# Performance work log

Measured on AMD Instinct MI355X. Metric: run time of the kernel, lower is better.

The kernel has to match this reference:

```python
import jax, jax.numpy as jnp
import numpy as np

# Param packing order: [capacitance_x, capacitance_y] + for each direction in
# (ax, by, xy, yx, xx, yy): [conductance, mean, std, pot]  -> total 26 scalars.
_DIR = {"ax": 0, "by": 1, "xy": 2, "yx": 3, "xx": 4, "yy": 5}

B, T = 4096, 4096


def setup_inputs() -> dict:
    key = jax.random.key(0)
    inputs = jax.random.normal(key, (B, T, 2), dtype=jnp.float32)
    # initializer constants from the keras layer
    params = jnp.asarray([1.0, 1.0] + [0.001, 0.3, 3.0, 1.0] * 6, dtype=jnp.float32)
    return {"inputs": inputs, "params": params}


def reference(inputs, params):
    cap_x, cap_y = params[0], params[1]

    def syn(d, pre, post):
        i = 2 + 4 * _DIR[d]
        g, mean, std, pot = params[i], params[i + 1], params[i + 2], params[i + 3]
        return g * jax.nn.sigmoid(std * (pre - mean)) * (pot - post)

    def step(state, inp):
        x, y = state                      # each [B, 1]
        a, b = inp[:, :1], inp[:, 1:]     # each [B, 1]
        cur_x = syn("ax", a, x) + syn("yx", y, x) + syn("xx", x, x)
        cur_y = syn("by", b, y) + syn("xy", x, y) + syn("yy", y, y)
        x = x + cur_x / cap_x
        y = y + cur_y / cap_y
        out = jnp.concatenate((x, y), axis=-1)  # [B, 2]
        return (x, y), out

    bsz = inputs.shape[0]
    x0 = jnp.zeros((bsz, 1), inputs.dtype)
    y0 = jnp.ones((bsz, 1), inputs.dtype)   # initial state = concat(zeros, ones)
    _, outs = jax.lax.scan(step, (x0, y0), jnp.swapaxes(inputs, 0, 1))  # [T, B, 2]
    return jnp.swapaxes(outs, 0, 1)  # [B, T, 2]
```

## Files before the change

kernel.cpp:

```cpp
#include <hip/hip_runtime.h>

#define TLEN  4096
#define NROWS 4096
#define RPB   32
#define K     32
#define NC    (TLEN / K)
#define SGSL  (16 * 64)
#define STP   34
#define STSL  (64 * STP)
#define UN    8

__device__ __forceinline__ float fexp2(float x) { return __builtin_amdgcn_exp2f(x); }
__device__ __forceinline__ float frcp(float x)  { return __builtin_amdgcn_rcpf(x); }
__device__ __forceinline__ float sigz(float z)  { return frcp(1.0f + fexp2(z)); }

__device__ __forceinline__ float lane_swap1(float v) {
    int r = __builtin_amdgcn_update_dpp(0, __float_as_int(v), 0xB1, 0xF, 0xF, true);
    return __int_as_float(r);
}

__device__ void run_fast(const float* __restrict__ inp, const float* __restrict__ prm,
                         float* __restrict__ out,
                         float4* __restrict__ sgbuf,
                         float*  __restrict__ st) {
    const int tid  = threadIdx.x;
    const int wid  = tid >> 6;
    const int lane = tid & 63;
    const int R0   = blockIdx.x * RPB;
    const float L2E = 1.4426950408889634f;
    float2* __restrict__ out2 = (float2*)out;

    if (wid == 1) {
        const int row = lane >> 1, dir = lane & 1;
        const float sd = dir ? prm[8] : prm[4];
        const float mn = dir ? prm[7] : prm[3];
        const float c1 = -sd * L2E, c0 = sd * mn * L2E;
        const float gA = dir ? (prm[6] / prm[1]) : (prm[2] / prm[0]);
        const float P  = gA * (dir ? prm[9] : prm[5]);
        const float Gn = -gA;
        const float4* __restrict__ src = (const float4*)inp + (size_t)(R0 + row) * (TLEN / 2);

        auto produce = [&](int c) {
            float4* sl = sgbuf + ((c & 1) ? SGSL : 0);
            const int base = c * 16;
#pragma unroll
            for (int j = 0; j < 16; ++j) {
                float4 v = src[base + j];
                float p0 = dir ? v.y : v.x;
                float p1 = dir ? v.w : v.z;
                float s0 = sigz(__builtin_fmaf(c1, p0, c0));
                float s1 = sigz(__builtin_fmaf(c1, p1, c0));
                float4 o; o.x = Gn * s0; o.y = P * s0;
                          o.z = Gn * s1; o.w = P * s1;
                sl[j * 64 + lane] = o;
            }
        };

        produce(0);
        __syncthreads();
        for (int c = 0; c < NC; ++c) {
            if (c + 1 < NC) produce(c + 1);
            __syncthreads();
        }
    } else if (wid == 2) {
        auto flush = [&](int c) {
            const float* sl = st + ((c & 1) ? STSL : 0);
            const int col = lane & 31;
#pragma unroll
            for (int j = 0; j < 16; ++j) {
                int ro = 2 * j + (lane >> 5);
                float2 v;
                v.x = sl[(2 * ro)     * STP + col];
                v.y = sl[(2 * ro + 1) * STP + col];
                out2[(size_t)(R0 + ro) * TLEN + (size_t)c * K + col] = v;
            }
        };

        __syncthreads();
        for (int c = 0; c < NC; ++c) {
            if (c >= 1) flush(c - 1);
            __syncthreads();
        }
        flush(NC - 1);
    } else {
        const int par = lane & 1;
        const int sfB = par ? 22 : 18, t2B = par ? 10 : 14;
        const float ic  = 1.0f / prm[par];
        const float g1  = prm[sfB] * ic, P1 = g1 * prm[sfB + 3], Gn1 = -g1;
        const float g2  = prm[t2B] * ic, P2 = g2 * prm[t2B + 3], Gn2 = -g2;
        const float sdz = prm[sfB + 2];
        const float c1s = -sdz * L2E, c0s = sdz * prm[sfB + 1] * L2E;

        float x   = par ? 1.0f : 0.0f;
        float sig = sigz(__builtin_fmaf(c1s, x, c0s));
        float u   = __builtin_fmaf(-sig, sig, sig);

        auto resync = [&]() {
            sig = sigz(__builtin_fmaf(c1s, x, c0s));
            u   = __builtin_fmaf(-sig, sig, sig);
        };

        __syncthreads();
        for (int c = 0; c < NC; ++c) {
            const float4* lb = sgbuf + ((c & 1) ? SGSL : 0);
            float* wp = st + ((c & 1) ? STSL : 0) + lane * STP;
            float4 f0 = lb[lane];
            float4 f1 = lb[64 + lane];
#pragma unroll
            for (int tp = 0; tp < 16; ++tp) {
                float4 f = f0; f0 = f1;
                if (tp < 14) f1 = lb[(tp + 2) * 64 + lane];
                float m   = __builtin_fmaf(f.x, x, f.y);
                float t1v = __builtin_fmaf(Gn1, x, P1);
                float t2v = __builtin_fmaf(Gn2, x, P2);
                float b2  = __builtin_fmaf(sig, t1v, m);
                float sc  = lane_swap1(sig);
                float dxa = __builtin_fmaf(sc, t2v, b2);
                x = x + dxa;
                float xa  = x;
                float dza = sdz * dxa;
                sig = __builtin_fmaf(u, dza, sig);
                float m2   = __builtin_fmaf(f.z, x, f.w);
                float t1v2 = __builtin_fmaf(Gn1, x, P1);
                float t2v2 = __builtin_fmaf(Gn2, x, P2);
                float b22  = __builtin_fmaf(sig, t1v2, m2);
                float sc2  = lane_swap1(sig);
                float dxb  = __builtin_fmaf(sc2, t2v2, b22);
                x = x + dxb;
                float dzb = sdz * dxb;
                sig = __builtin_fmaf(u, dzb, sig);
                u   = __builtin_fmaf(-sig, sig, sig);
                float2 w2; w2.x = xa; w2.y = x;
                *(float2*)(wp + 2 * tp) = w2;
                if (tp == 7) resync();
            }
            resync();
            __syncthreads();
        }
    }
}

struct LaneConst {
    float c1_in, c0_in, c1_sf, c0_sf, c1_ot, c0_ot;
    float gS_in, gS_cr, gS_sf, gP_in, gP_cr, gP_sf;
};

__device__ __forceinline__ float do_step_exact(float s, float pre_in, const LaneConst& k) {
    float sig_in = sigz(__builtin_fmaf(k.c1_in, pre_in, k.c0_in));
    float sig_sf = sigz(__builtin_fmaf(k.c1_sf, s, k.c0_sf));
    float sig_ot = sigz(__builtin_fmaf(k.c1_ot, s, k.c0_ot));
    float sig_cr = lane_swap1(sig_ot);
    float S = __builtin_fmaf(k.gS_in, sig_in, __builtin_fmaf(k.gS_cr, sig_cr, k.gS_sf * sig_sf));
    float P = __builtin_fmaf(k.gP_in, sig_in, __builtin_fmaf(k.gP_cr, sig_cr, k.gP_sf * sig_sf));
    return s + __builtin_fmaf(S, -s, P);
}

__device__ void run_exact(const float* __restrict__ inp, const float* __restrict__ prm,
                          float* __restrict__ out) {
    const int tid = blockIdx.x * 192 + threadIdx.x;
    const int row = tid >> 1;
    if (row >= NROWS) return;
    const int par = tid & 1;
    const float L2E = 1.4426950408889634f;
    const int inB = par ? 6 : 2, sfB = par ? 22 : 18, otB = par ? 14 : 10, crB = par ? 10 : 14;
    const float invc = 1.0f / prm[par];
    LaneConst k;
    float sd = prm[inB + 2], mn = prm[inB + 1];
    k.c1_in = -sd * L2E; k.c0_in = sd * mn * L2E;
    sd = prm[sfB + 2]; mn = prm[sfB + 1];
    k.c1_sf = -sd * L2E; k.c0_sf = sd * mn * L2E;
    sd = prm[otB + 2]; mn = prm[otB + 1];
    k.c1_ot = -sd * L2E; k.c0_ot = sd * mn * L2E;
    k.gS_in = prm[inB] * invc; k.gP_in = k.gS_in * prm[inB + 3];
    k.gS_sf = prm[sfB] * invc; k.gP_sf = k.gS_sf * prm[sfB + 3];
    k.gS_cr = prm[crB] * invc; k.gP_cr = k.gS_cr * prm[crB + 3];

    const float4* __restrict__ src = (const float4*)inp + (size_t)row * (TLEN / 2);
    float* __restrict__ dst = out + (size_t)row * (TLEN * 2) + par;
    float s = par ? 1.0f : 0.0f;

    float4 cur[UN], nxt[UN];
#pragma unroll
    for (int j = 0; j < UN; ++j) cur[j] = src[j];
    const int NIT = TLEN / (2 * UN);
    for (int it = 0; it < NIT; ++it) {
        if (it + 1 < NIT) {
#pragma unroll
            for (int j = 0; j < UN; ++j) nxt[j] = src[(it + 1) * UN + j];
        }
        float* dptr = dst + it * (UN * 4);
#pragma unroll
        for (int j = 0; j < UN; ++j) {
            float4 f = cur[j];
            s = do_step_exact(s, par ? f.y : f.x, k);
            dptr[j * 4] = s;
            s = do_step_exact(s, par ? f.w : f.z, k);
            dptr[j * 4 + 2] = s;
        }
#pragma unroll
        for (int j = 0; j < UN; ++j) cur[j] = nxt[j];
    }
}

__global__ __launch_bounds__(192, 1)
void memcell_scan(const float* __restrict__ inp, const float* __restrict__ prm,
                  float* __restrict__ out) {
    __shared__ float4 sgbuf[2 * SGSL];
    __shared__ float  st[2 * STSL];

    const bool shared = (prm[11] == prm[19]) && (prm[12] == prm[20]) &&
                        (prm[15] == prm[23]) && (prm[16] == prm[24]);
    const float capx = prm[0], capy = prm[1];
    const bool gpos = prm[2] >= 0.f && prm[6] >= 0.f && prm[10] >= 0.f &&
                      prm[14] >= 0.f && prm[18] >= 0.f && prm[22] >= 0.f &&
                      capx > 0.f && capy > 0.f;
    const float sx = (prm[2] + prm[14] + prm[18]) / capx;
    const float sy = (prm[6] + prm[10] + prm[22]) / capy;
    const float lox = fminf(0.f, fminf(prm[5], fminf(prm[17], prm[21])));
    const float hix = fmaxf(0.f, fmaxf(prm[5], fmaxf(prm[17], prm[21])));
    const float loy = fminf(1.f, fminf(prm[9], fminf(prm[13], prm[25])));
    const float hiy = fmaxf(1.f, fmaxf(prm[9], fmaxf(prm[13], prm[25])));
    const float wbx = prm[20] * sx * (hix - lox), wby = prm[24] * sy * (hiy - loy);
    const float zmx = prm[20] * fmaxf(fabsf(lox - prm[19]), fabsf(hix - prm[19]));
    const float zmy = prm[24] * fmaxf(fabsf(loy - prm[23]), fabsf(hiy - prm[23]));
    const bool fast = shared && gpos && sx <= 0.25f && sy <= 0.25f &&
                      wbx <= 0.02f && wby <= 0.02f && zmx <= 20.f && zmy <= 20.f;
    if (fast) {
        run_fast(inp, prm, out, sgbuf, st);
    } else {
        run_exact(inp, prm, out);
    }
}

extern "C" void kernel_launch(void* const* d_in, const int* in_sizes, int n_in,
                              void* d_out, int out_size, void* d_ws, size_t ws_size,
                              hipStream_t stream) {
    (void)in_sizes; (void)n_in; (void)d_ws; (void)ws_size; (void)out_size;
    const float* inp = (const float*)d_in[0];
    const float* prm = (const float*)d_in[1];
    float* out = (float*)d_out;
    memcell_scan<<<dim3(NROWS / RPB), dim3(192), 0, stream>>>(inp, prm, out);
}
```

Baseline: 372.8 us.

## Merge producer and flush waves, prefetch inputs into LDS asynchronously

Folds the output-flush wave into the sigmoid-producer wave, so the block shrinks from three waves to two. Input chunks are now prefetched two steps ahead with global_load_lds straight into a double-buffered LDS staging area, in place of synchronous per-lane global loads. The aim is to hide input load latency behind compute and to cut per-block wave overhead. The cost is that one wave now does both the input and output work per chunk, which could lengthen its critical path relative to the scan wave. The exact fallback path's launch indexing is also changed to 128 threads per block.

```diff
diff --git a/kernel.cpp b/kernel.cpp
--- a/kernel.cpp
+++ b/kernel.cpp
@@ -5,6 +5,7 @@
 #define RPB   32
 #define K     32
 #define NC    (TLEN / K)
+#define IBSL  (8 * 64)
 #define SGSL  (16 * 64)
 #define STP   34
 #define STSL  (64 * STP)
@@ -19,8 +20,19 @@
     return __int_as_float(r);
 }
 
+__device__ __forceinline__ void gload_lds16(const float4* g, float4* l) {
+    __builtin_amdgcn_global_load_lds((const __attribute__((address_space(1))) void*)g,
+                                     (__attribute__((address_space(3))) void*)l,
+                                     16, 0, 0);
+}
+__device__ __forceinline__ void fence_vm0() {
+    __builtin_amdgcn_s_waitcnt(0x0f70);
+    __builtin_amdgcn_sched_barrier(0);
+}
+
 __device__ void run_fast(const float* __restrict__ inp, const float* __restrict__ prm,
                          float* __restrict__ out,
+                         float4* __restrict__ ibuf,
                          float4* __restrict__ sgbuf,
                          float*  __restrict__ st) {
     const int tid  = threadIdx.x;
@@ -38,31 +50,31 @@
         const float gA = dir ? (prm[6] / prm[1]) : (prm[2] / prm[0]);
         const float P  = gA * (dir ? prm[9] : prm[5]);
         const float Gn = -gA;
-        const float4* __restrict__ src = (const float4*)inp + (size_t)(R0 + row) * (TLEN / 2);
-
+
+        const float4* gbase = (const float4*)inp
+                            + (size_t)(R0 + (lane & 31)) * (TLEN / 2) + (lane >> 5);
+        auto kick = [&](int c) {
+            float4* lb = ibuf + ((c & 1) ? IBSL : 0);
+            const float4* gp = gbase + c * 16;
+#pragma unroll
+            for (int j = 0; j < 8; ++j)
+                gload_lds16(gp + 2 * j, lb + (j << 6));
+        };
         auto produce = [&](int c) {
+            const float4* ib = ibuf + ((c & 1) ? IBSL : 0);
             float4* sl = sgbuf + ((c & 1) ? SGSL : 0);
-            const int base = c * 16;
-#pragma unroll
-            for (int j = 0; j < 16; ++j) {
-                float4 v = src[base + j];
+#pragma unroll
+            for (int g = 0; g < 16; ++g) {
+                float4 v = ib[(g >> 1) * 64 + (g & 1) * 32 + row];
                 float p0 = dir ? v.y : v.x;
                 float p1 = dir ? v.w : v.z;
                 float s0 = sigz(__builtin_fmaf(c1, p0, c0));
                 float s1 = sigz(__builtin_fmaf(c1, p1, c0));
                 float4 o; o.x = Gn * s0; o.y = P * s0;
                           o.z = Gn * s1; o.w = P * s1;
-                sl[j * 64 + lane] = o;
-            }
-        };
-
-        produce(0);
-        __syncthreads();
-        for (int c = 0; c < NC; ++c) {
-            if (c + 1 < NC) produce(c + 1);
-            __syncthreads();
-        }
-    } else if (wid == 2) {
+                sl[g * 64 + lane] = o;
+            }
+        };
         auto flush = [&](int c) {
             const float* sl = st + ((c & 1) ? STSL : 0);
             const int col = lane & 31;
@@ -76,9 +88,18 @@
             }
         };
 
+        kick(0);
+        fence_vm0();
+        produce(0);
+        kick(1);
         __syncthreads();
         for (int c = 0; c < NC; ++c) {
-            if (c >= 1) flush(c - 1);
+            if (c + 1 < NC) {
+                fence_vm0();
+                produce(c + 1);
+            }
+            if (c + 2 < NC) kick(c + 2);
+            if (c >= 1)     flush(c - 1);
             __syncthreads();
         }
         flush(NC - 1);
@@ -157,7 +178,7 @@
 
 __device__ void run_exact(const float* __restrict__ inp, const float* __restrict__ prm,
                           float* __restrict__ out) {
-    const int tid = blockIdx.x * 192 + threadIdx.x;
+    const int tid = blockIdx.x * 128 + threadIdx.x;
     const int row = tid >> 1;
     if (row >= NROWS) return;
     const int par = tid & 1;
@@ -202,9 +223,10 @@
     }
 }
 
-__global__ __launch_bounds__(192, 1)
+__global__ __launch_bounds__(128, 1)
 void memcell_scan(const float* __restrict__ inp, const float* __restrict__ prm,
                   float* __restrict__ out) {
+    __shared__ float4 ibuf[2 * IBSL];
     __shared__ float4 sgbuf[2 * SGSL];
     __shared__ float  st[2 * STSL];
 
@@ -226,7 +248,7 @@
     const bool fast = shared && gpos && sx <= 0.25f && sy <= 0.25f &&
                       wbx <= 0.02f && wby <= 0.02f && zmx <= 20.f && zmy <= 20.f;
     if (fast) {
-        run_fast(inp, prm, out, sgbuf, st);
+        run_fast(inp, prm, out, ibuf, sgbuf, st);
     } else {
         run_exact(inp, prm, out);
     }
@@ -239,5 +261,5 @@
     const float* inp = (const float*)d_in[0];
     const float* prm = (const float*)d_in[1];
     float* out = (float*)d_out;
-    memcell_scan<<<dim3(NROWS / RPB), dim3(192), 0, stream>>>(inp, prm, out);
-}
+    memcell_scan<<<dim3(NROWS / RPB), dim3(128), 0, stream>>>(inp, prm, out);
+}
```

Result: slower. 403.4 us (+8.2%).
